# Optimization experiments

Hardware: AMD Instinct MI355X
Metric: run time of the kernel (lower is better)

## Reference

```python
import jax, jax.numpy as jnp
import numpy as np

N_ATOMS = 100_000
N_BONDS = 200_000
MAX_NB = 6
HIDDEN = 300
ATOM_FD = 133
BOND_FD = 147
DEPTH = 3
ATOMS_PER_MOL = 20
N_MOLS = N_ATOMS // ATOMS_PER_MOL


def setup_inputs() -> dict:
    key = jax.random.key(0)
    ks = jax.random.split(key, 9)
    f_atoms = jax.random.normal(ks[0], (N_ATOMS, ATOM_FD), dtype=jnp.float32)
    f_bonds = jax.random.normal(ks[1], (N_BONDS, BOND_FD), dtype=jnp.float32)
    a2b = jax.random.randint(ks[2], (N_ATOMS, MAX_NB), 0, N_BONDS, dtype=jnp.int32)
    b2a = jax.random.randint(ks[3], (N_BONDS,), 0, N_ATOMS, dtype=jnp.int32)
    b2revb = jax.random.randint(ks[4], (N_BONDS,), 0, N_BONDS, dtype=jnp.int32)
    mol_ids = (jnp.arange(N_ATOMS, dtype=jnp.int32) // ATOMS_PER_MOL).astype(jnp.int32)
    W_i = jax.random.normal(ks[5], (BOND_FD, HIDDEN), dtype=jnp.float32) * 0.05
    W_h = jax.random.normal(ks[6], (HIDDEN, HIDDEN), dtype=jnp.float32) * 0.05
    W_o = jax.random.normal(ks[7], (ATOM_FD + HIDDEN, HIDDEN), dtype=jnp.float32) * 0.05
    b_o = jax.random.normal(ks[8], (HIDDEN,), dtype=jnp.float32) * 0.05
    return {"f_atoms": f_atoms, "f_bonds": f_bonds, "a2b": a2b, "b2a": b2a,
            "b2revb": b2revb, "mol_ids": mol_ids, "W_i": W_i, "W_h": W_h,
            "W_o": W_o, "b_o": b_o}


def reference(f_atoms, f_bonds, a2b, b2a, b2revb, mol_ids, W_i, W_h, W_o, b_o):
    # input = W_i(f_bonds); message = act(input)
    inp = f_bonds @ W_i                     # [n_bonds, H]
    message = jax.nn.relu(inp)
    for _ in range(DEPTH - 1):
        # padded-neighbor gather + sum over incoming bonds per atom
        a_message = message[a2b].sum(axis=1)          # [n_atoms, H]
        # forward gather minus reverse-bond message
        m = a_message[b2a] - message[b2revb]          # [n_bonds, H]
        message = jax.nn.relu(inp + m @ W_h)          # (dropout p=0 omitted)
    # final atom readout
    a_message = message[a2b].sum(axis=1)              # [n_atoms, H]
    a_input = jnp.concatenate([f_atoms, a_message], axis=1)  # [n_atoms, atom_fd+H]
    atom_hiddens = jax.nn.relu(a_input @ W_o + b_o)   # [n_atoms, H]
    # 'mean' pooling over each molecule's atoms (contiguous equal-size scopes)
    mol_sums = jax.ops.segment_sum(atom_hiddens, mol_ids, num_segments=N_MOLS)
    return mol_sums / ATOMS_PER_MOL                   # [n_mols, H]
```

## Files before the change

### kernel.cpp

```cpp
#include <hip/hip_runtime.h>
#include <hip/hip_bf16.h>
#include <hip/hip_fp8.h>

#define N_ATOMS 100000
#define N_BONDS 200000
#define MAX_NB 6
#define HIDDEN 300
#define HP 320
#define CH 40
#define ATOM_FD 133
#define BOND_FD 147
#define N_MOLS 5000
#define APM 20

#define NT32 10
#define KKI32 10
#define KKH32 20
#define KKO32 28

using bf16 = __hip_bfloat16;
typedef __attribute__((ext_vector_type(8))) short short8v;
typedef __attribute__((ext_vector_type(4))) float float4v;
typedef __attribute__((ext_vector_type(16))) float float16v;
typedef unsigned int u32;
typedef unsigned short u16;
typedef unsigned char u8;

__device__ __forceinline__ float us2f(u16 u) {
    union { u32 i; float f; } v; v.i = ((u32)u) << 16; return v.f;
}
__device__ __forceinline__ u16 f2us(float f) {
    bf16 h = __float2bfloat16(f);
    return *(u16*)&h;
}
__device__ __forceinline__ u32 pack2(float a, float b) {
    return (u32)f2us(a) | ((u32)f2us(b) << 16);
}
__device__ __forceinline__ uint2 pack4(const float4v& a) {
    uint2 o; o.x = pack2(a[0], a[1]); o.y = pack2(a[2], a[3]); return o;
}
__device__ __forceinline__ u32 relu2(u32 u) {
    u32 r = (u & 0x80000000u) ? (u & 0x0000ffffu) : u;
    r = (r & 0x8000u) ? (r & 0xffff0000u) : r;
    return r;
}
__device__ __forceinline__ uint4 relu8(uint4 u) {
    u.x = relu2(u.x); u.y = relu2(u.y); u.z = relu2(u.z); u.w = relu2(u.w);
    return u;
}

#if defined(__has_builtin)
#if __has_builtin(__builtin_amdgcn_cvt_f32_fp8) && __has_builtin(__builtin_amdgcn_cvt_pk_fp8_f32)
#define HW_FP8 1
#endif
#endif

__device__ __forceinline__ void f8x4_to_f32(u32 p, float* o) {
#ifdef HW_FP8
    o[0] = __builtin_amdgcn_cvt_f32_fp8(p, 0);
    o[1] = __builtin_amdgcn_cvt_f32_fp8(p, 1);
    o[2] = __builtin_amdgcn_cvt_f32_fp8(p, 2);
    o[3] = __builtin_amdgcn_cvt_f32_fp8(p, 3);
#else
#pragma unroll
    for (int i = 0; i < 4; ++i) {
        __hip_fp8_e4m3 h; h.__x = (u8)(p >> (8 * i));
        o[i] = (float)h;
    }
#endif
}
__device__ __forceinline__ u32 f32x4_to_f8(float a, float b, float c, float d) {
#ifdef HW_FP8
    u32 r = __builtin_amdgcn_cvt_pk_fp8_f32(a, b, 0u, false);
    r = __builtin_amdgcn_cvt_pk_fp8_f32(c, d, r, true);
    return r;
#else
    __hip_fp8_e4m3 ha(a), hb(b), hc(c), hd(d);
    return (u32)ha.__x | ((u32)hb.__x << 8) | ((u32)hc.__x << 16) | ((u32)hd.__x << 24);
#endif
}
__device__ __forceinline__ void f8x16_to_f32(uint4 u, float* o) {
    f8x4_to_f32(u.x, o); f8x4_to_f32(u.y, o + 4);
    f8x4_to_f32(u.z, o + 8); f8x4_to_f32(u.w, o + 12);
}

__global__ __launch_bounds__(64) void pack_w32(const float* __restrict__ src,
                                               short* __restrict__ dst,
                                               int Ksrc, int mode) {
    int kk = blockIdx.x / NT32, nt = blockIdx.x % NT32;
    int lane = threadIdx.x;
    int col = nt * 32 + (lane & 31);
#pragma unroll
    for (int j = 0; j < 8; ++j) {
        int k = kk * 16 + (lane >> 5) * 8 + j;
        float v = 0.f;
        if (k < Ksrc && col < HIDDEN) {
            int krow = k;
            if (mode == 2) krow = (k < HIDDEN) ? (ATOM_FD + k) : (k - HIDDEN);
            v = src[krow * HIDDEN + col];
        }
        dst[(((kk * NT32 + nt) << 6) + lane) * 8 + j] = (short)f2us(v);
    }
}

__global__ __launch_bounds__(320) void k1_input(const float* __restrict__ fb,
                                                const short8v* __restrict__ WiP,
                                                u16* __restrict__ inp) {
    __shared__ __align__(16) char sm[32 * 640];
    const int tid = threadIdx.x;
    const long base = (long)blockIdx.x * 32;
    const float4* src4 = (const float4*)(fb + base * BOND_FD);
#pragma unroll
    for (int it = 0; it < 4; ++it) {
        int idx = tid + it * 320;
        if (idx < 1176) {
            float4 v = src4[idx];
            int f = idx * 4;
#pragma unroll
            for (int e = 0; e < 4; ++e) {
                int g = f + e;
                int r = g / BOND_FD, c = g - r * BOND_FD;
                int byte = r * 320 + c * 2;
                *(u16*)(sm + (byte ^ ((r & 7) << 4))) = f2us(((const float*)&v)[e]);
            }
        }
    }
    for (int i = tid; i < 32 * 13; i += 320) {
        int r = i / 13, c = BOND_FD + i % 13;
        int byte = r * 320 + c * 2;
        *(u16*)(sm + (byte ^ ((r & 7) << 4))) = 0;
    }
    __syncthreads();

    const int lane = tid & 63, wave = tid >> 6;
    const int row = lane & 31, hi = lane >> 5;
    const int nt0 = wave * 2;
    float16v acc0, acc1;
#pragma unroll
    for (int q = 0; q < 16; ++q) { acc0[q] = 0.f; acc1[q] = 0.f; }
    for (int kk = 0; kk < KKI32; ++kk) {
        int byte = row * 320 + kk * 32 + hi * 16;
        short8v a = *(const short8v*)(sm + (byte ^ ((row & 7) << 4)));
        short8v w0 = WiP[((kk * NT32 + nt0) << 6) + lane];
        short8v w1 = WiP[((kk * NT32 + nt0 + 1) << 6) + lane];
        acc0 = __builtin_amdgcn_mfma_f32_32x32x16_bf16(w0, a, acc0, 0, 0, 0);
        acc1 = __builtin_amdgcn_mfma_f32_32x32x16_bf16(w1, a, acc1, 0, 0, 0);
    }
    __syncthreads();
#pragma unroll
    for (int q = 0; q < 4; ++q) {
        float4v v0, v1;
#pragma unroll
        for (int d = 0; d < 4; ++d) { v0[d] = acc0[4 * q + d]; v1[d] = acc1[4 * q + d]; }
        int swz = (row & 7) << 4;
        int b0 = row * 640 + nt0 * 64 + q * 16 + hi * 8;
        int b1 = b0 + 64;
        *(uint2*)(sm + (b0 ^ swz)) = pack4(v0);
        *(uint2*)(sm + (b1 ^ swz)) = pack4(v1);
    }
    __syncthreads();
#pragma unroll
    for (int it = 0; it < 4; ++it) {
        int i = tid + it * 320;
        int r = i / CH, c = i % CH;
        int byte = r * 640 + c * 16;
        uint4 v = *(const uint4*)(sm + (byte ^ ((r & 7) << 4)));
        ((uint4*)(inp + (base + r) * HP))[c] = v;
    }
}

template<int SRCBF>
__global__ __launch_bounds__(256, 8) void k2_gather(const void* __restrict__ srcv,
                                                    const int* __restrict__ a2b,
                                                    u8* __restrict__ dst) {
    int id = blockIdx.x * 256 + threadIdx.x;
    int atom = id / 20, c = id % 20;
    if (atom >= N_ATOMS) return;
    const int* nb = a2b + atom * MAX_NB;
    float s[16];
#pragma unroll
    for (int q = 0; q < 16; ++q) s[q] = 0.f;
#pragma unroll
    for (int j = 0; j < MAX_NB; ++j) {
        int b = nb[j];
        if (SRCBF) {
            const uint4* rp = (const uint4*)((const u16*)srcv + (long)b * HP);
            uint4 u0 = relu8(rp[2 * c]);
            uint4 u1 = relu8(rp[2 * c + 1]);
            s[0] += us2f(u0.x & 0xffff); s[1] += us2f(u0.x >> 16);
            s[2] += us2f(u0.y & 0xffff); s[3] += us2f(u0.y >> 16);
            s[4] += us2f(u0.z & 0xffff); s[5] += us2f(u0.z >> 16);
            s[6] += us2f(u0.w & 0xffff); s[7] += us2f(u0.w >> 16);
            s[8]  += us2f(u1.x & 0xffff); s[9]  += us2f(u1.x >> 16);
            s[10] += us2f(u1.y & 0xffff); s[11] += us2f(u1.y >> 16);
            s[12] += us2f(u1.z & 0xffff); s[13] += us2f(u1.z >> 16);
            s[14] += us2f(u1.w & 0xffff); s[15] += us2f(u1.w >> 16);
        } else {
            uint4 u = ((const uint4*)((const u8*)srcv + (long)b * 320))[c];
            float v[16];
            f8x16_to_f32(u, v);
#pragma unroll
            for (int q = 0; q < 16; ++q) s[q] += v[q];
        }
    }
    uint4 o;
    o.x = f32x4_to_f8(s[0], s[1], s[2], s[3]);
    o.y = f32x4_to_f8(s[4], s[5], s[6], s[7]);
    o.z = f32x4_to_f8(s[8], s[9], s[10], s[11]);
    o.w = f32x4_to_f8(s[12], s[13], s[14], s[15]);
    ((uint4*)(dst + (long)atom * 320))[c] = o;
}

template<int SRCBF>
__global__ __launch_bounds__(320) void kzf_update(const u16* __restrict__ inp,
                                                  const u8* __restrict__ AM,
                                                  const void* __restrict__ msgsrcv,
                                                  const int* __restrict__ b2a,
                                                  const int* __restrict__ b2revb,
                                                  const short8v* __restrict__ WhP,
                                                  u8* __restrict__ msgdst) {
    __shared__ __align__(16) char sm[32 * 640];
    const int tid = threadIdx.x;
    const long base = (long)blockIdx.x * 32;

#pragma unroll
    for (int it = 0; it < 2; ++it) {
        int i = tid + it * 320;
        int r = i / 20, c = i % 20;
        long b = base + r;
        int ia = b2a[b], ir = b2revb[b];
        uint4 ua = ((const uint4*)(AM + (long)ia * 320))[c];
        float av[16];
        f8x16_to_f32(ua, av);
        float mv[16];
        if (SRCBF) {
            const uint4* rp = (const uint4*)((const u16*)msgsrcv + (long)ir * HP);
            uint4 u0 = relu8(rp[2 * c]);
            uint4 u1 = relu8(rp[2 * c + 1]);
            mv[0] = us2f(u0.x & 0xffff); mv[1] = us2f(u0.x >> 16);
            mv[2] = us2f(u0.y & 0xffff); mv[3] = us2f(u0.y >> 16);
            mv[4] = us2f(u0.z & 0xffff); mv[5] = us2f(u0.z >> 16);
            mv[6] = us2f(u0.w & 0xffff); mv[7] = us2f(u0.w >> 16);
            mv[8]  = us2f(u1.x & 0xffff); mv[9]  = us2f(u1.x >> 16);
            mv[10] = us2f(u1.y & 0xffff); mv[11] = us2f(u1.y >> 16);
            mv[12] = us2f(u1.z & 0xffff); mv[13] = us2f(u1.z >> 16);
            mv[14] = us2f(u1.w & 0xffff); mv[15] = us2f(u1.w >> 16);
        } else {
            uint4 um = ((const uint4*)((const u8*)msgsrcv + (long)ir * 320))[c];
            f8x16_to_f32(um, mv);
        }
        uint4 o0, o1;
        o0.x = pack2(av[0] - mv[0], av[1] - mv[1]);
        o0.y = pack2(av[2] - mv[2], av[3] - mv[3]);
        o0.z = pack2(av[4] - mv[4], av[5] - mv[5]);
        o0.w = pack2(av[6] - mv[6], av[7] - mv[7]);
        o1.x = pack2(av[8] - mv[8], av[9] - mv[9]);
        o1.y = pack2(av[10] - mv[10], av[11] - mv[11]);
        o1.z = pack2(av[12] - mv[12], av[13] - mv[13]);
        o1.w = pack2(av[14] - mv[14], av[15] - mv[15]);
        int byte = r * 640 + c * 32;
        int swz = (r & 7) << 4;
        *(uint4*)(sm + (byte ^ swz)) = o0;
        *(uint4*)(sm + ((byte + 16) ^ swz)) = o1;
    }
    __syncthreads();

    const int lane = tid & 63, wave = tid >> 6;
    const int row = lane & 31, hi = lane >> 5;
    const int nt0 = wave * 2;
    float16v acc0, acc1;
#pragma unroll
    for (int q = 0; q < 16; ++q) { acc0[q] = 0.f; acc1[q] = 0.f; }
    for (int kk = 0; kk < KKH32; ++kk) {
        int byte = row * 640 + kk * 32 + hi * 16;
        short8v a = *(const short8v*)(sm + (byte ^ ((row & 7) << 4)));
        short8v w0 = WhP[((kk * NT32 + nt0) << 6) + lane];
        short8v w1 = WhP[((kk * NT32 + nt0 + 1) << 6) + lane];
        acc0 = __builtin_amdgcn_mfma_f32_32x32x16_bf16(w0, a, acc0, 0, 0, 0);
        acc1 = __builtin_amdgcn_mfma_f32_32x32x16_bf16(w1, a, acc1, 0, 0, 0);
    }
    __syncthreads();
#pragma unroll
    for (int t = 0; t < 2; ++t) {
#pragma unroll
        for (int q = 0; q < 4; ++q) {
            int colb = (nt0 + t) * 32 + q * 8 + hi * 4;
            uint2 u = *(const uint2*)(inp + (base + row) * HP + colb);
            float a0 = (t == 0 ? acc0[4 * q + 0] : acc1[4 * q + 0]);
            float a1 = (t == 0 ? acc0[4 * q + 1] : acc1[4 * q + 1]);
            float a2 = (t == 0 ? acc0[4 * q + 2] : acc1[4 * q + 2]);
            float a3 = (t == 0 ? acc0[4 * q + 3] : acc1[4 * q + 3]);
            float v0 = fmaxf(a0 + us2f(u.x & 0xffff), 0.f);
            float v1 = fmaxf(a1 + us2f(u.x >> 16), 0.f);
            float v2 = fmaxf(a2 + us2f(u.y & 0xffff), 0.f);
            float v3 = fmaxf(a3 + us2f(u.y >> 16), 0.f);
            *(u32*)(sm + row * 336 + colb) = f32x4_to_f8(v0, v1, v2, v3);
        }
    }
    __syncthreads();
#pragma unroll
    for (int it = 0; it < 2; ++it) {
        int i = tid + it * 320;
        int r = i / 20, c = i % 20;
        uint4 v = *(const uint4*)(sm + r * 336 + c * 16);
        ((uint4*)(msgdst + (base + r) * 320))[c] = v;
    }
}

__global__ __launch_bounds__(640, 8) void k4_gemm(const float* __restrict__ fa,
                                                  const u8* __restrict__ AM,
                                                  const short8v* __restrict__ WoP,
                                                  const float* __restrict__ bo,
                                                  u16* __restrict__ ah) {
    __shared__ __align__(16) char sm[32 * 896];
    const int tid = threadIdx.x;
    const long base = (long)blockIdx.x * 32;
    if (tid < 608) {
        int row = tid / 19, c = tid % 19;
        uint4 u = ((const uint4*)(AM + (base + row) * 320))[c];
        float v[16];
        f8x16_to_f32(u, v);
        uint4 o0, o1;
        o0.x = pack2(v[0], v[1]);  o0.y = pack2(v[2], v[3]);
        o0.z = pack2(v[4], v[5]);  o0.w = pack2(v[6], v[7]);
        o1.x = pack2(v[8], v[9]);  o1.y = pack2(v[10], v[11]);
        o1.z = pack2(v[12], v[13]); o1.w = pack2(v[14], v[15]);
        int byte = row * 896 + c * 32;
        int swz = (row & 7) << 4;
        *(uint4*)(sm + (byte ^ swz)) = o0;
        if (c < 18) {
            *(uint4*)(sm + ((byte + 16) ^ swz)) = o1;
        } else {
            *(uint2*)(sm + ((byte + 16) ^ swz)) = make_uint2(o1.x, o1.y);
        }
    }
    for (int i = tid; i < 32 * 148; i += 640) {
        int row = i / 148, c2 = i % 148;
        float v = (c2 < ATOM_FD) ? fa[(base + row) * ATOM_FD + c2] : 0.f;
        int byte = row * 896 + (HIDDEN + c2) * 2;
        *(u16*)(sm + (byte ^ ((row & 7) << 4))) = f2us(v);
    }
    __syncthreads();

    const int lane = tid & 63, wave = tid >> 6;
    const int row = lane & 31, hi = lane >> 5;
    float16v acc;
#pragma unroll
    for (int q = 0; q < 16; ++q) acc[q] = 0.f;
    for (int kk = 0; kk < KKO32; ++kk) {
        int byte = row * 896 + kk * 32 + hi * 16;
        short8v a = *(const short8v*)(sm + (byte ^ ((row & 7) << 4)));
        short8v w = WoP[((kk * NT32 + wave) << 6) + lane];
        acc = __builtin_amdgcn_mfma_f32_32x32x16_bf16(w, a, acc, 0, 0, 0);
    }
    __syncthreads();
#pragma unroll
    for (int q = 0; q < 4; ++q) {
        int colb = wave * 32 + q * 8 + hi * 4;
        float4v v;
#pragma unroll
        for (int d = 0; d < 4; ++d) {
            float bias = (colb + d < HIDDEN) ? bo[colb + d] : 0.f;
            v[d] = fmaxf(acc[4 * q + d] + bias, 0.f);
        }
        int byte = row * 640 + colb * 2;
        *(uint2*)(sm + (byte ^ ((row & 7) << 4))) = pack4(v);
    }
    __syncthreads();
#pragma unroll
    for (int it = 0; it < 2; ++it) {
        int i = tid + it * 640;
        if (i < 1280) {
            int r = i / CH, c = i % CH;
            int byte = r * 640 + c * 16;
            uint4 v = *(const uint4*)(sm + (byte ^ ((r & 7) << 4)));
            ((uint4*)(ah + (base + r) * HP))[c] = v;
        }
    }
}

__global__ __launch_bounds__(320) void k5_pool(const u16* __restrict__ ah,
                                               float* __restrict__ out) {
    const int h = threadIdx.x;
    const int mol = blockIdx.x;
    if (h >= HIDDEN) return;
    float s = 0.f;
#pragma unroll
    for (int a = 0; a < APM; ++a)
        s += us2f(ah[((long)mol * APM + a) * HP + h]);
    out[(long)mol * HIDDEN + h] = s * (1.f / APM);
}

extern "C" void kernel_launch(void* const* d_in, const int* in_sizes, int n_in,
                              void* d_out, int out_size, void* d_ws, size_t ws_size,
                              hipStream_t stream) {
    const float* f_atoms = (const float*)d_in[0];
    const float* f_bonds = (const float*)d_in[1];
    const int* a2b = (const int*)d_in[2];
    const int* b2a = (const int*)d_in[3];
    const int* b2revb = (const int*)d_in[4];
    const float* Wi = (const float*)d_in[6];
    const float* Wh = (const float*)d_in[7];
    const float* Wo = (const float*)d_in[8];
    const float* bo = (const float*)d_in[9];
    float* out = (float*)d_out;

    char* ws = (char*)d_ws;
    size_t off = 0;
    auto alloc = [&](size_t bytes) {
        void* p = ws + off;
        off = (off + bytes + 255) & ~(size_t)255;
        return p;
    };
    u16* inp  = (u16*)alloc((size_t)N_BONDS * HP * sizeof(u16));
    u8* msgA  = (u8*)alloc((size_t)N_BONDS * 320);
    u8* msgB  = (u8*)alloc((size_t)N_BONDS * 320);
    u8* AM    = (u8*)alloc((size_t)N_ATOMS * 320);
    short* WiP32 = (short*)alloc((size_t)KKI32 * NT32 * 64 * 8 * sizeof(short));
    short* WhP32 = (short*)alloc((size_t)KKH32 * NT32 * 64 * 8 * sizeof(short));
    short* WoP32 = (short*)alloc((size_t)KKO32 * NT32 * 64 * 8 * sizeof(short));
    u16* ah = (u16*)msgA;

    pack_w32<<<KKI32 * NT32, 64, 0, stream>>>(Wi, WiP32, BOND_FD, 0);
    pack_w32<<<KKH32 * NT32, 64, 0, stream>>>(Wh, WhP32, HIDDEN, 0);
    pack_w32<<<KKO32 * NT32, 64, 0, stream>>>(Wo, WoP32, ATOM_FD + HIDDEN, 2);

    k1_input<<<N_BONDS / 32, 320, 0, stream>>>(f_bonds, (const short8v*)WiP32, inp);

    const int g2 = (N_ATOMS * 20 + 255) / 256;
    k2_gather<1><<<g2, 256, 0, stream>>>(inp, a2b, AM);
    kzf_update<1><<<N_BONDS / 32, 320, 0, stream>>>(inp, AM, inp, b2a, b2revb,
                                                    (const short8v*)WhP32, msgA);
    k2_gather<0><<<g2, 256, 0, stream>>>(msgA, a2b, AM);
    kzf_update<0><<<N_BONDS / 32, 320, 0, stream>>>(inp, AM, msgA, b2a, b2revb,
                                                    (const short8v*)WhP32, msgB);
    k2_gather<0><<<g2, 256, 0, stream>>>(msgB, a2b, AM);
    k4_gemm<<<N_ATOMS / 32, 640, 0, stream>>>(f_atoms, AM,
                                              (const short8v*)WoP32, bo, ah);
    k5_pool<<<N_MOLS, 320, 0, stream>>>(ah, out);
}
```

Measured before the change: 495.2 us.

## Fuse final neighbor gather into readout GEMM and widen fp8 gather

The final a2b gather-sum is moved into the readout GEMM kernel, so each block sums six fp8 neighbor message rows straight into shared memory and the separate gather launch plus the AM write/read round trip go away. The fp8 gather kernel now has each thread handle 32 bytes (two uint4) per atom instead of 16, which halves the thread count. The f_atoms staging loads float4 vectors instead of scalar floats and pads the extra columns separately. The fused GEMM prologue now does irregular gathers before its MFMA loop, which may lengthen that kernel.

```diff
diff --git a/kernel.cpp b/kernel.cpp
--- a/kernel.cpp
+++ b/kernel.cpp
@@ -174,16 +174,16 @@
                                                     const int* __restrict__ a2b,
                                                     u8* __restrict__ dst) {
     int id = blockIdx.x * 256 + threadIdx.x;
-    int atom = id / 20, c = id % 20;
-    if (atom >= N_ATOMS) return;
-    const int* nb = a2b + atom * MAX_NB;
-    float s[16];
-#pragma unroll
-    for (int q = 0; q < 16; ++q) s[q] = 0.f;
-#pragma unroll
-    for (int j = 0; j < MAX_NB; ++j) {
-        int b = nb[j];
-        if (SRCBF) {
+    if (SRCBF) {
+        int atom = id / 20, c = id % 20;
+        if (atom >= N_ATOMS) return;
+        const int* nb = a2b + atom * MAX_NB;
+        float s[16];
+#pragma unroll
+        for (int q = 0; q < 16; ++q) s[q] = 0.f;
+#pragma unroll
+        for (int j = 0; j < MAX_NB; ++j) {
+            int b = nb[j];
             const uint4* rp = (const uint4*)((const u16*)srcv + (long)b * HP);
             uint4 u0 = relu8(rp[2 * c]);
             uint4 u1 = relu8(rp[2 * c + 1]);
@@ -195,20 +195,46 @@
             s[10] += us2f(u1.y & 0xffff); s[11] += us2f(u1.y >> 16);
             s[12] += us2f(u1.z & 0xffff); s[13] += us2f(u1.z >> 16);
             s[14] += us2f(u1.w & 0xffff); s[15] += us2f(u1.w >> 16);
-        } else {
-            uint4 u = ((const uint4*)((const u8*)srcv + (long)b * 320))[c];
+        }
+        uint4 o;
+        o.x = f32x4_to_f8(s[0], s[1], s[2], s[3]);
+        o.y = f32x4_to_f8(s[4], s[5], s[6], s[7]);
+        o.z = f32x4_to_f8(s[8], s[9], s[10], s[11]);
+        o.w = f32x4_to_f8(s[12], s[13], s[14], s[15]);
+        ((uint4*)(dst + (long)atom * 320))[c] = o;
+    } else {
+        int atom = id / 10, c2 = id % 10;
+        if (atom >= N_ATOMS) return;
+        const int* nb = a2b + atom * MAX_NB;
+        float s[32];
+#pragma unroll
+        for (int q = 0; q < 32; ++q) s[q] = 0.f;
+#pragma unroll
+        for (int j = 0; j < MAX_NB; ++j) {
+            const uint4* rp = (const uint4*)((const u8*)srcv + (long)nb[j] * 320);
+            uint4 u0 = rp[2 * c2];
+            uint4 u1 = rp[2 * c2 + 1];
             float v[16];
-            f8x16_to_f32(u, v);
+            f8x16_to_f32(u0, v);
 #pragma unroll
             for (int q = 0; q < 16; ++q) s[q] += v[q];
-        }
-    }
-    uint4 o;
-    o.x = f32x4_to_f8(s[0], s[1], s[2], s[3]);
-    o.y = f32x4_to_f8(s[4], s[5], s[6], s[7]);
-    o.z = f32x4_to_f8(s[8], s[9], s[10], s[11]);
-    o.w = f32x4_to_f8(s[12], s[13], s[14], s[15]);
-    ((uint4*)(dst + (long)atom * 320))[c] = o;
+            f8x16_to_f32(u1, v);
+#pragma unroll
+            for (int q = 0; q < 16; ++q) s[16 + q] += v[q];
+        }
+        uint4 o0, o1;
+        o0.x = f32x4_to_f8(s[0], s[1], s[2], s[3]);
+        o0.y = f32x4_to_f8(s[4], s[5], s[6], s[7]);
+        o0.z = f32x4_to_f8(s[8], s[9], s[10], s[11]);
+        o0.w = f32x4_to_f8(s[12], s[13], s[14], s[15]);
+        o1.x = f32x4_to_f8(s[16], s[17], s[18], s[19]);
+        o1.y = f32x4_to_f8(s[20], s[21], s[22], s[23]);
+        o1.z = f32x4_to_f8(s[24], s[25], s[26], s[27]);
+        o1.w = f32x4_to_f8(s[28], s[29], s[30], s[31]);
+        uint4* dp = (uint4*)(dst + (long)atom * 320);
+        dp[2 * c2] = o0;
+        dp[2 * c2 + 1] = o1;
+    }
 }
 
 template<int SRCBF>
@@ -308,7 +334,8 @@
 }
 
 __global__ __launch_bounds__(640, 8) void k4_gemm(const float* __restrict__ fa,
-                                                  const u8* __restrict__ AM,
+                                                  const u8* __restrict__ msg,
+                                                  const int* __restrict__ a2b,
                                                   const short8v* __restrict__ WoP,
                                                   const float* __restrict__ bo,
                                                   u16* __restrict__ ah) {
@@ -317,14 +344,24 @@
     const long base = (long)blockIdx.x * 32;
     if (tid < 608) {
         int row = tid / 19, c = tid % 19;
-        uint4 u = ((const uint4*)(AM + (base + row) * 320))[c];
-        float v[16];
-        f8x16_to_f32(u, v);
+        long atom = base + row;
+        const int* nb = a2b + atom * MAX_NB;
+        float s[16];
+#pragma unroll
+        for (int q = 0; q < 16; ++q) s[q] = 0.f;
+#pragma unroll
+        for (int j = 0; j < MAX_NB; ++j) {
+            uint4 u = ((const uint4*)(msg + (long)nb[j] * 320))[c];
+            float v[16];
+            f8x16_to_f32(u, v);
+#pragma unroll
+            for (int q = 0; q < 16; ++q) s[q] += v[q];
+        }
         uint4 o0, o1;
-        o0.x = pack2(v[0], v[1]);  o0.y = pack2(v[2], v[3]);
-        o0.z = pack2(v[4], v[5]);  o0.w = pack2(v[6], v[7]);
-        o1.x = pack2(v[8], v[9]);  o1.y = pack2(v[10], v[11]);
-        o1.z = pack2(v[12], v[13]); o1.w = pack2(v[14], v[15]);
+        o0.x = pack2(s[0], s[1]);  o0.y = pack2(s[2], s[3]);
+        o0.z = pack2(s[4], s[5]);  o0.w = pack2(s[6], s[7]);
+        o1.x = pack2(s[8], s[9]);  o1.y = pack2(s[10], s[11]);
+        o1.z = pack2(s[12], s[13]); o1.w = pack2(s[14], s[15]);
         int byte = row * 896 + c * 32;
         int swz = (row & 7) << 4;
         *(uint4*)(sm + (byte ^ swz)) = o0;
@@ -334,11 +371,26 @@
             *(uint2*)(sm + ((byte + 16) ^ swz)) = make_uint2(o1.x, o1.y);
         }
     }
-    for (int i = tid; i < 32 * 148; i += 640) {
-        int row = i / 148, c2 = i % 148;
-        float v = (c2 < ATOM_FD) ? fa[(base + row) * ATOM_FD + c2] : 0.f;
-        int byte = row * 896 + (HIDDEN + c2) * 2;
-        *(u16*)(sm + (byte ^ ((row & 7) << 4))) = f2us(v);
+    const float4* src4 = (const float4*)(fa + base * ATOM_FD);
+#pragma unroll
+    for (int it = 0; it < 2; ++it) {
+        int idx = tid + it * 640;
+        if (idx < 1064) {
+            float4 v = src4[idx];
+            int f = idx * 4;
+#pragma unroll
+            for (int e = 0; e < 4; ++e) {
+                int g = f + e;
+                int r = g / ATOM_FD, c2 = g - r * ATOM_FD;
+                int byte = r * 896 + (HIDDEN + c2) * 2;
+                *(u16*)(sm + (byte ^ ((r & 7) << 4))) = f2us(((const float*)&v)[e]);
+            }
+        }
+    }
+    if (tid < 480) {
+        int r = tid / 15, c2 = ATOM_FD + tid % 15;
+        int byte = r * 896 + (HIDDEN + c2) * 2;
+        *(u16*)(sm + (byte ^ ((r & 7) << 4))) = 0;
     }
     __syncthreads();
 
@@ -427,15 +479,15 @@
 
     k1_input<<<N_BONDS / 32, 320, 0, stream>>>(f_bonds, (const short8v*)WiP32, inp);
 
-    const int g2 = (N_ATOMS * 20 + 255) / 256;
-    k2_gather<1><<<g2, 256, 0, stream>>>(inp, a2b, AM);
+    const int g2a = (N_ATOMS * 20 + 255) / 256;
+    k2_gather<1><<<g2a, 256, 0, stream>>>(inp, a2b, AM);
     kzf_update<1><<<N_BONDS / 32, 320, 0, stream>>>(inp, AM, inp, b2a, b2revb,
                                                     (const short8v*)WhP32, msgA);
-    k2_gather<0><<<g2, 256, 0, stream>>>(msgA, a2b, AM);
+    const int g2b = (N_ATOMS * 10 + 255) / 256;
+    k2_gather<0><<<g2b, 256, 0, stream>>>(msgA, a2b, AM);
     kzf_update<0><<<N_BONDS / 32, 320, 0, stream>>>(inp, AM, msgA, b2a, b2revb,
                                                     (const short8v*)WhP32, msgB);
-    k2_gather<0><<<g2, 256, 0, stream>>>(msgB, a2b, AM);
-    k4_gemm<<<N_ATOMS / 32, 640, 0, stream>>>(f_atoms, AM,
+    k4_gemm<<<N_ATOMS / 32, 640, 0, stream>>>(f_atoms, msgB, a2b,
                                               (const short8v*)WoP32, bo, ah);
     k5_pool<<<N_MOLS, 320, 0, stream>>>(ah, out);
 }
```

Result: faster. 461.3 us (-6.8%).
